# Performance work log

Measured on AMD Instinct MI355X. Metric: run time of the kernel, lower is better.

## Reference

```python
import jax, jax.numpy as jnp
import numpy as np

B = 2_000_000   # batch of affine transforms
N = 3           # spatial ndims -> flattened transform has N*(N+1)=12 entries


def setup_inputs() -> dict:
    key = jax.random.key(0)
    # small shifts so that identity + shift is always invertible
    trf = jax.random.normal(key, (B, N * (N + 1)), dtype=jnp.float32) * 0.1
    return {"trf": trf}


def reference(trf):
    """Batched equivalent of tf.map_fn(_single_invert, trf).

    Per sample: lift flattened (N,N+1) shift to an (N+1,N+1) matrix over the
    identity, invert it, and convert back to a flattened shift.
    """
    b = trf.shape[0]
    eye = jnp.eye(N + 1, dtype=trf.dtype)
    # affine_shift_to_identity: (b, N, N+1) -> pad zero row -> add identity
    mat = trf.reshape(b, N, N + 1)
    full = jnp.concatenate(
        [mat, jnp.zeros((b, 1, N + 1), dtype=trf.dtype)], axis=1
    ) + eye                                  # (b, N+1, N+1)
    inv = jnp.linalg.inv(full)               # batched tiny inversions
    # affine_identity_to_shift: subtract identity, drop last row, flatten
    shift = (inv - eye)[:, :N, :]            # (b, N, N+1)
    return shift.reshape(b, N * (N + 1))
```

## Files before the change

kernel.cpp:

```cpp
#include <hip/hip_runtime.h>


__global__ __launch_bounds__(256) void invert_affine_kernel(
    const float4* __restrict__ in, float4* __restrict__ out, int b) {
  int i = blockIdx.x * blockDim.x + threadIdx.x;
  if (i >= b) return;

  float4 r0 = in[3 * i + 0];
  float4 r1 = in[3 * i + 1];
  float4 r2 = in[3 * i + 2];

  float a00 = r0.x + 1.0f, a01 = r0.y,        a02 = r0.z,        t0 = r0.w;
  float a10 = r1.x,        a11 = r1.y + 1.0f, a12 = r1.z,        t1 = r1.w;
  float a20 = r2.x,        a21 = r2.y,        a22 = r2.z + 1.0f, t2 = r2.w;

  float b00 = a11 * a22 - a12 * a21;
  float b01 = a02 * a21 - a01 * a22;
  float b02 = a01 * a12 - a02 * a11;
  float b10 = a12 * a20 - a10 * a22;
  float b11 = a00 * a22 - a02 * a20;
  float b12 = a02 * a10 - a00 * a12;
  float b20 = a10 * a21 - a11 * a20;
  float b21 = a01 * a20 - a00 * a21;
  float b22 = a00 * a11 - a01 * a10;

  float det = a00 * b00 + a01 * b10 + a02 * b20;
  float rdet = 1.0f / det;

  b00 *= rdet; b01 *= rdet; b02 *= rdet;
  b10 *= rdet; b11 *= rdet; b12 *= rdet;
  b20 *= rdet; b21 *= rdet; b22 *= rdet;

  float4 o0, o1, o2;
  o0.x = b00 - 1.0f; o0.y = b01;        o0.z = b02;
  o0.w = -(b00 * t0 + b01 * t1 + b02 * t2);
  o1.x = b10;        o1.y = b11 - 1.0f; o1.z = b12;
  o1.w = -(b10 * t0 + b11 * t1 + b12 * t2);
  o2.x = b20;        o2.y = b21;        o2.z = b22 - 1.0f;
  o2.w = -(b20 * t0 + b21 * t1 + b22 * t2);

  out[3 * i + 0] = o0;
  out[3 * i + 1] = o1;
  out[3 * i + 2] = o2;
}

extern "C" void kernel_launch(void* const* d_in, const int* in_sizes, int n_in,
                              void* d_out, int out_size, void* d_ws, size_t ws_size,
                              hipStream_t stream) {
  const float4* trf = (const float4*)d_in[0];
  float4* out = (float4*)d_out;
  int b = in_sizes[0] / 12;
  const int threads = 256;
  int blocks = (b + threads - 1) / threads;
  invert_affine_kernel<<<blocks, threads, 0, stream>>>(trf, out, b);
}
```

Before: 171.3 us.

## Stage per-block transforms through LDS for coalesced global loads and stores

Each block now loads its 256 samples' float4 rows into shared memory with contiguous, fully coalesced accesses. It inverts each matrix from LDS and writes the results back to LDS, then stores them to global memory coalesced. Before this, each thread read three float4s at a stride of 48 bytes, which spread every wavefront's accesses across memory. The change adds two block barriers, LDS traffic and possible bank conflicts on the strided LDS reads, and also sets a minimum of 8 blocks per CU in launch bounds.

```diff
diff --git a/kernel.cpp b/kernel.cpp
--- a/kernel.cpp
+++ b/kernel.cpp
@@ -1,47 +1,68 @@
 #include <hip/hip_runtime.h>
 
 
-__global__ __launch_bounds__(256) void invert_affine_kernel(
+__global__ __launch_bounds__(256, 8) void invert_affine_kernel(
     const float4* __restrict__ in, float4* __restrict__ out, int b) {
-  int i = blockIdx.x * blockDim.x + threadIdx.x;
-  if (i >= b) return;
+  __shared__ float4 buf[768];
 
-  float4 r0 = in[3 * i + 0];
-  float4 r1 = in[3 * i + 1];
-  float4 r2 = in[3 * i + 2];
+  const int tid = threadIdx.x;
+  const int base_s = blockIdx.x * 256;
+  const int base_f4 = base_s * 3;
+  const int n_f4 = b * 3;
 
-  float a00 = r0.x + 1.0f, a01 = r0.y,        a02 = r0.z,        t0 = r0.w;
-  float a10 = r1.x,        a11 = r1.y + 1.0f, a12 = r1.z,        t1 = r1.w;
-  float a20 = r2.x,        a21 = r2.y,        a22 = r2.z + 1.0f, t2 = r2.w;
+#pragma unroll
+  for (int k = 0; k < 3; ++k) {
+    int idx = base_f4 + k * 256 + tid;
+    if (idx < n_f4) buf[k * 256 + tid] = in[idx];
+  }
+  __syncthreads();
 
-  float b00 = a11 * a22 - a12 * a21;
-  float b01 = a02 * a21 - a01 * a22;
-  float b02 = a01 * a12 - a02 * a11;
-  float b10 = a12 * a20 - a10 * a22;
-  float b11 = a00 * a22 - a02 * a20;
-  float b12 = a02 * a10 - a00 * a12;
-  float b20 = a10 * a21 - a11 * a20;
-  float b21 = a01 * a20 - a00 * a21;
-  float b22 = a00 * a11 - a01 * a10;
+  const int s = base_s + tid;
+  if (s < b) {
+    float4 r0 = buf[tid * 3 + 0];
+    float4 r1 = buf[tid * 3 + 1];
+    float4 r2 = buf[tid * 3 + 2];
 
-  float det = a00 * b00 + a01 * b10 + a02 * b20;
-  float rdet = 1.0f / det;
+    float a00 = r0.x + 1.0f, a01 = r0.y,        a02 = r0.z,        t0 = r0.w;
+    float a10 = r1.x,        a11 = r1.y + 1.0f, a12 = r1.z,        t1 = r1.w;
+    float a20 = r2.x,        a21 = r2.y,        a22 = r2.z + 1.0f, t2 = r2.w;
 
-  b00 *= rdet; b01 *= rdet; b02 *= rdet;
-  b10 *= rdet; b11 *= rdet; b12 *= rdet;
-  b20 *= rdet; b21 *= rdet; b22 *= rdet;
+    float b00 = a11 * a22 - a12 * a21;
+    float b01 = a02 * a21 - a01 * a22;
+    float b02 = a01 * a12 - a02 * a11;
+    float b10 = a12 * a20 - a10 * a22;
+    float b11 = a00 * a22 - a02 * a20;
+    float b12 = a02 * a10 - a00 * a12;
+    float b20 = a10 * a21 - a11 * a20;
+    float b21 = a01 * a20 - a00 * a21;
+    float b22 = a00 * a11 - a01 * a10;
 
-  float4 o0, o1, o2;
-  o0.x = b00 - 1.0f; o0.y = b01;        o0.z = b02;
-  o0.w = -(b00 * t0 + b01 * t1 + b02 * t2);
-  o1.x = b10;        o1.y = b11 - 1.0f; o1.z = b12;
-  o1.w = -(b10 * t0 + b11 * t1 + b12 * t2);
-  o2.x = b20;        o2.y = b21;        o2.z = b22 - 1.0f;
-  o2.w = -(b20 * t0 + b21 * t1 + b22 * t2);
+    float det = a00 * b00 + a01 * b10 + a02 * b20;
+    float rdet = 1.0f / det;
 
-  out[3 * i + 0] = o0;
-  out[3 * i + 1] = o1;
-  out[3 * i + 2] = o2;
+    b00 *= rdet; b01 *= rdet; b02 *= rdet;
+    b10 *= rdet; b11 *= rdet; b12 *= rdet;
+    b20 *= rdet; b21 *= rdet; b22 *= rdet;
+
+    float4 o0, o1, o2;
+    o0.x = b00 - 1.0f; o0.y = b01;        o0.z = b02;
+    o0.w = -(b00 * t0 + b01 * t1 + b02 * t2);
+    o1.x = b10;        o1.y = b11 - 1.0f; o1.z = b12;
+    o1.w = -(b10 * t0 + b11 * t1 + b12 * t2);
+    o2.x = b20;        o2.y = b21;        o2.z = b22 - 1.0f;
+    o2.w = -(b20 * t0 + b21 * t1 + b22 * t2);
+
+    buf[tid * 3 + 0] = o0;
+    buf[tid * 3 + 1] = o1;
+    buf[tid * 3 + 2] = o2;
+  }
+  __syncthreads();
+
+#pragma unroll
+  for (int k = 0; k < 3; ++k) {
+    int idx = base_f4 + k * 256 + tid;
+    if (idx < n_f4) out[idx] = buf[k * 256 + tid];
+  }
 }
 
 extern "C" void kernel_launch(void* const* d_in, const int* in_sizes, int n_in,
```

Measured after the change: 168.2 us. About the same (-1.8%).

## Process four transforms per thread with grid-stride loop and fixed grid

Applied to the files above, without the earlier changes.

Each thread now loads 12 consecutive float4s (four transforms), inverts them in registers, and stores 12 float4s, inside a grid-stride loop over a fixed 1024x256 grid. The goal is more memory parallelism per thread and less launch and tail overhead. The cost is a strided per-thread access pattern: lanes sit 192 bytes apart, so each wave's loads are less coalesced. Register pressure also rises.

```diff
diff --git a/kernel.cpp b/kernel.cpp
--- a/kernel.cpp
+++ b/kernel.cpp
@@ -3,45 +3,89 @@
 
 __global__ __launch_bounds__(256) void invert_affine_kernel(
     const float4* __restrict__ in, float4* __restrict__ out, int b) {
-  int i = blockIdx.x * blockDim.x + threadIdx.x;
-  if (i >= b) return;
+  const int tid = blockIdx.x * blockDim.x + threadIdx.x;
+  const int nthreads = gridDim.x * blockDim.x;
+  const int ngroups = (b + 3) >> 2;
 
-  float4 r0 = in[3 * i + 0];
-  float4 r1 = in[3 * i + 1];
-  float4 r2 = in[3 * i + 2];
+  for (int g = tid; g < ngroups; g += nthreads) {
+    const int f4base = g * 12;
+    const int rem = b - g * 4;
+    float4 v[12];
 
-  float a00 = r0.x + 1.0f, a01 = r0.y,        a02 = r0.z,        t0 = r0.w;
-  float a10 = r1.x,        a11 = r1.y + 1.0f, a12 = r1.z,        t1 = r1.w;
-  float a20 = r2.x,        a21 = r2.y,        a22 = r2.z + 1.0f, t2 = r2.w;
+    if (rem >= 4) {
+#pragma unroll
+      for (int k = 0; k < 12; ++k) v[k] = in[f4base + k];
 
-  float b00 = a11 * a22 - a12 * a21;
-  float b01 = a02 * a21 - a01 * a22;
-  float b02 = a01 * a12 - a02 * a11;
-  float b10 = a12 * a20 - a10 * a22;
-  float b11 = a00 * a22 - a02 * a20;
-  float b12 = a02 * a10 - a00 * a12;
-  float b20 = a10 * a21 - a11 * a20;
-  float b21 = a01 * a20 - a00 * a21;
-  float b22 = a00 * a11 - a01 * a10;
+#pragma unroll
+      for (int j = 0; j < 4; ++j) {
+        float4 r0 = v[3 * j + 0], r1 = v[3 * j + 1], r2 = v[3 * j + 2];
 
-  float det = a00 * b00 + a01 * b10 + a02 * b20;
-  float rdet = 1.0f / det;
+        float a00 = r0.x + 1.0f, a01 = r0.y,        a02 = r0.z,        t0 = r0.w;
+        float a10 = r1.x,        a11 = r1.y + 1.0f, a12 = r1.z,        t1 = r1.w;
+        float a20 = r2.x,        a21 = r2.y,        a22 = r2.z + 1.0f, t2 = r2.w;
 
-  b00 *= rdet; b01 *= rdet; b02 *= rdet;
-  b10 *= rdet; b11 *= rdet; b12 *= rdet;
-  b20 *= rdet; b21 *= rdet; b22 *= rdet;
+        float b00 = a11 * a22 - a12 * a21;
+        float b01 = a02 * a21 - a01 * a22;
+        float b02 = a01 * a12 - a02 * a11;
+        float b10 = a12 * a20 - a10 * a22;
+        float b11 = a00 * a22 - a02 * a20;
+        float b12 = a02 * a10 - a00 * a12;
+        float b20 = a10 * a21 - a11 * a20;
+        float b21 = a01 * a20 - a00 * a21;
+        float b22 = a00 * a11 - a01 * a10;
 
-  float4 o0, o1, o2;
-  o0.x = b00 - 1.0f; o0.y = b01;        o0.z = b02;
-  o0.w = -(b00 * t0 + b01 * t1 + b02 * t2);
-  o1.x = b10;        o1.y = b11 - 1.0f; o1.z = b12;
-  o1.w = -(b10 * t0 + b11 * t1 + b12 * t2);
-  o2.x = b20;        o2.y = b21;        o2.z = b22 - 1.0f;
-  o2.w = -(b20 * t0 + b21 * t1 + b22 * t2);
+        float det = a00 * b00 + a01 * b10 + a02 * b20;
+        float rdet = 1.0f / det;
 
-  out[3 * i + 0] = o0;
-  out[3 * i + 1] = o1;
-  out[3 * i + 2] = o2;
+        b00 *= rdet; b01 *= rdet; b02 *= rdet;
+        b10 *= rdet; b11 *= rdet; b12 *= rdet;
+        b20 *= rdet; b21 *= rdet; b22 *= rdet;
+
+        v[3 * j + 0] = make_float4(b00 - 1.0f, b01, b02,
+                                   -(b00 * t0 + b01 * t1 + b02 * t2));
+        v[3 * j + 1] = make_float4(b10, b11 - 1.0f, b12,
+                                   -(b10 * t0 + b11 * t1 + b12 * t2));
+        v[3 * j + 2] = make_float4(b20, b21, b22 - 1.0f,
+                                   -(b20 * t0 + b21 * t1 + b22 * t2));
+      }
+
+#pragma unroll
+      for (int k = 0; k < 12; ++k) out[f4base + k] = v[k];
+    } else {
+      for (int j = 0; j < rem; ++j) {
+        const int fb = f4base + 3 * j;
+        float4 r0 = in[fb + 0], r1 = in[fb + 1], r2 = in[fb + 2];
+
+        float a00 = r0.x + 1.0f, a01 = r0.y,        a02 = r0.z,        t0 = r0.w;
+        float a10 = r1.x,        a11 = r1.y + 1.0f, a12 = r1.z,        t1 = r1.w;
+        float a20 = r2.x,        a21 = r2.y,        a22 = r2.z + 1.0f, t2 = r2.w;
+
+        float b00 = a11 * a22 - a12 * a21;
+        float b01 = a02 * a21 - a01 * a22;
+        float b02 = a01 * a12 - a02 * a11;
+        float b10 = a12 * a20 - a10 * a22;
+        float b11 = a00 * a22 - a02 * a20;
+        float b12 = a02 * a10 - a00 * a12;
+        float b20 = a10 * a21 - a11 * a20;
+        float b21 = a01 * a20 - a00 * a21;
+        float b22 = a00 * a11 - a01 * a10;
+
+        float det = a00 * b00 + a01 * b10 + a02 * b20;
+        float rdet = 1.0f / det;
+
+        b00 *= rdet; b01 *= rdet; b02 *= rdet;
+        b10 *= rdet; b11 *= rdet; b12 *= rdet;
+        b20 *= rdet; b21 *= rdet; b22 *= rdet;
+
+        out[fb + 0] = make_float4(b00 - 1.0f, b01, b02,
+                                  -(b00 * t0 + b01 * t1 + b02 * t2));
+        out[fb + 1] = make_float4(b10, b11 - 1.0f, b12,
+                                  -(b10 * t0 + b11 * t1 + b12 * t2));
+        out[fb + 2] = make_float4(b20, b21, b22 - 1.0f,
+                                  -(b20 * t0 + b21 * t1 + b22 * t2));
+      }
+    }
+  }
 }
 
 extern "C" void kernel_launch(void* const* d_in, const int* in_sizes, int n_in,
@@ -50,7 +94,5 @@
   const float4* trf = (const float4*)d_in[0];
   float4* out = (float4*)d_out;
   int b = in_sizes[0] / 12;
-  const int threads = 256;
-  int blocks = (b + threads - 1) / threads;
-  invert_affine_kernel<<<blocks, threads, 0, stream>>>(trf, out, b);
+  invert_affine_kernel<<<1024, 256, 0, stream>>>(trf, out, b);
 }
```

New measurement: 190.0 us. 10.9% more time.
